# Performance work log

Hardware: AMD Instinct MI355X
Metric: run time of the kernel (lower is better)

The kernel has to match this reference:

```python
import jax, jax.numpy as jnp
import numpy as np

NEG = -9e15  # mask value used by dense GAT-style implementations
ALPHA = 0.1  # leaky_relu negative slope (init arg)
DENSITY = 0.05  # sparsity of the incidence/adjacency operator


def setup_inputs() -> dict:
    key = jax.random.key(0)
    ks = jax.random.split(key, 7)
    n_s, n_t = 8192, 4096
    s_in = t_in = 128
    s_out = t_out = 64
    H = 4
    input1 = jax.random.normal(ks[0], (n_s, s_in), dtype=jnp.float32)
    input2 = jax.random.normal(ks[1], (n_t, t_in), dtype=jnp.float32)
    A_opt = (jax.random.uniform(ks[2], (n_t, n_s)) < DENSITY).astype(jnp.float32)
    # per-head params, stacked on leading head axis (math identical to num_heads separate layers)
    Ws = jax.random.normal(ks[3], (H, s_in, t_out), dtype=jnp.float32) * (1.0 / np.sqrt(s_in))
    Wt = jax.random.normal(ks[4], (H, t_in, s_out), dtype=jnp.float32) * (1.0 / np.sqrt(t_in))
    a_src = jax.random.normal(ks[5], (H, t_out), dtype=jnp.float32) * 0.1
    a_tgt = jax.random.normal(ks[6], (H, s_out), dtype=jnp.float32) * 0.1
    return {"input1": input1, "input2": input2, "A_opt": A_opt,
            "Ws": Ws, "Wt": Wt, "a_src": a_src, "a_tgt": a_tgt}


def _forward(input1, input2, A_opt, Ws, Wt, a_src, a_tgt):
    # hs: source feats projected to target_out space; ht: target feats -> source_out space
    hs = jnp.einsum('si,hio->hso', input1, Ws)          # [H, n_s, t_out]
    ht = jnp.einsum('ti,hio->hto', input2, Wt)          # [H, n_t, s_out]
    # additive GAT score, broadcast over the [n_t, n_s] grid
    e = jax.nn.leaky_relu(
        jnp.einsum('hto,ho->ht', ht, a_tgt)[:, :, None]
        + jnp.einsum('hso,ho->hs', hs, a_src)[:, None, :],
        negative_slope=ALPHA)                            # [H, n_t, n_s]
    mask = (A_opt != 0.0)[None]                          # [1, n_t, n_s]
    e_masked = jnp.where(mask, e, NEG)
    attn_ts = jax.nn.softmax(e_masked, axis=-1)          # normalize over source cells
    attn_st = jax.nn.softmax(e_masked, axis=-2)          # normalize over target cells
    h_ts = jax.nn.elu(jnp.einsum('hts,hso->hto', attn_ts, hs))  # [H, n_t, t_out]
    h_st = jax.nn.elu(jnp.einsum('hts,hto->hso', attn_st, ht))  # [H, n_s, s_out]
    # concatenate heads along feature dim (concatenate=True)
    out_st = jnp.transpose(h_st, (1, 0, 2)).reshape(input1.shape[0], -1)  # [n_s, H*s_out]
    out_ts = jnp.transpose(h_ts, (1, 0, 2)).reshape(input2.shape[0], -1)  # [n_t, H*t_out]
    return out_st, out_ts


def reference(input1, input2, A_opt, Ws, Wt, a_src, a_tgt):
    return _forward(input1, input2, A_opt, Ws, Wt, a_src, a_tgt)
```

## Files before the change

### kernel.cpp

```cpp
#include <hip/hip_runtime.h>
#include <hip/hip_bf16.h>

#define H 4
#define NS 8192
#define NT 4096
#define DIN 128
#define DOUT 64
#define ROW_CAP 1024
#define COL_CAP 512
#define NEGBIG -3.0e38f

typedef unsigned uint4_vt __attribute__((ext_vector_type(4)));

__device__ __forceinline__ float lrelu(float x) { return x >= 0.f ? x : 0.1f * x; }
__device__ __forceinline__ float eluf(float x) { return x > 0.f ? x : expm1f(x); }

__device__ __forceinline__ float waveMax(float v) {
    for (int off = 32; off > 0; off >>= 1) v = fmaxf(v, __shfl_xor(v, off, 64));
    return v;
}
__device__ __forceinline__ float waveSum(float v) {
    for (int off = 32; off > 0; off >>= 1) v += __shfl_xor(v, off, 64);
    return v;
}
__device__ __forceinline__ float rlane(float v, int l) {
    return __int_as_float(__builtin_amdgcn_readlane(__float_as_int(v), l));
}

__global__ __launch_bounds__(256) void proj_kernel(
    const float* __restrict__ X, const float* __restrict__ W,
    const float* __restrict__ a_vec, float* __restrict__ Hout,
    float* __restrict__ b_out, int N) {
    __shared__ float w_lds[DIN * DOUT];
    __shared__ float a_lds[16 * 129];
    const int h = blockIdx.y;
    const int row0 = blockIdx.x * 16;
    const int tid = threadIdx.x;

    const float* Wh = W + (size_t)h * DIN * DOUT;
    for (int i = tid; i < DIN * DOUT; i += 256) w_lds[i] = Wh[i];
    for (int i = tid; i < 16 * DIN; i += 256) {
        int r = i >> 7, c = i & 127;
        a_lds[r * 129 + c] = X[(size_t)(row0 + r) * DIN + c];
    }
    __syncthreads();

    const int fg = (tid & 15) * 4;
    const int r = tid >> 4;
    const float* ar = &a_lds[r * 129];
    float acc0 = 0.f, acc1 = 0.f, acc2 = 0.f, acc3 = 0.f;
#pragma unroll 8
    for (int i = 0; i < DIN; ++i) {
        float av = ar[i];
        float4 wv = *reinterpret_cast<const float4*>(&w_lds[i * DOUT + fg]);
        acc0 += av * wv.x; acc1 += av * wv.y; acc2 += av * wv.z; acc3 += av * wv.w;
    }
    const int s = row0 + r;
    float4 o = make_float4(acc0, acc1, acc2, acc3);
    *reinterpret_cast<float4*>(&Hout[((size_t)h * N + s) * DOUT + fg]) = o;

    const float* av = a_vec + h * DOUT + fg;
    float part = acc0 * av[0] + acc1 * av[1] + acc2 * av[2] + acc3 * av[3];
    for (int off = 8; off > 0; off >>= 1) part += __shfl_xor(part, off, 64);
    if ((tid & 15) == 0) b_out[(size_t)h * N + s] = part;
}

__global__ __launch_bounds__(256) void mask_kernel(
    const float* __restrict__ A,
    unsigned long long* __restrict__ mask_row,
    unsigned long long* __restrict__ mask_col) {
    __shared__ unsigned long long rowbits[64];
    const int s0 = blockIdx.x * 64;
    const int t0 = blockIdx.y * 64;
    const int lane = threadIdx.x & 63;
    const int w = threadIdx.x >> 6;
    for (int rr = w; rr < 64; rr += 4) {
        const int t = t0 + rr;
        float v = A[(size_t)t * NS + s0 + lane];
        unsigned long long word = __ballot(v != 0.0f);
        if (lane == 0) {
            mask_row[(size_t)t * (NS / 64) + (s0 >> 6)] = word;
            rowbits[rr] = word;
        }
    }
    __syncthreads();
    if (threadIdx.x < 64) {
        const int j = threadIdx.x;
        unsigned long long cw = 0;
        for (int rr = 0; rr < 64; ++rr) cw |= ((rowbits[rr] >> j) & 1ull) << rr;
        mask_col[(size_t)(s0 + j) * (NT / 64) + (t0 >> 6)] = cw;
    }
}

template <int NWORDS, int CAP>
__device__ __forceinline__ int wave_compact(
    const unsigned long long* __restrict__ mask, size_t word_base,
    unsigned* list, int lane) {
    int total = 0;
#pragma unroll
    for (int c = 0; c < NWORDS / 64; ++c) {
        unsigned long long wd = mask[word_base + c * 64 + lane];
        int cnt = __popcll(wd);
        int incl = cnt;
#pragma unroll
        for (int d = 1; d < 64; d <<= 1) {
            int v = __shfl_up(incl, d, 64);
            if (lane >= d) incl += v;
        }
        int off = total + incl - cnt;
        const unsigned base = (unsigned)(c * 64 + lane) * 64u;
        while (wd) {
            int b = __ffsll((long long)wd) - 1;
            if (off < CAP) list[off] = (base + (unsigned)b) << 8;
            ++off;
            wd &= wd - 1;
        }
        total += __shfl(incl, 63, 64);
    }
    int nnz = total > CAP ? CAP : total;
    int nk64 = (nnz + 63) & ~63;
    for (int j = nnz + lane; j < nk64; j += 64) list[j] = 0;
    return nnz;
}

template <int KMAX>
__device__ __forceinline__ float attn_core(
    const unsigned* __restrict__ list, int nnz,
    const float* __restrict__ bvec,
    float bias,
    const float* __restrict__ src,
    int lane) {
    const int nk = (nnz + 63) >> 6;
    float wreg[KMAX];

    float m = NEGBIG;
#pragma unroll
    for (int k = 0; k < KMAX; ++k) {
        if (k >= nk) break;
        int j = (k << 6) + lane;
        float p = NEGBIG;
        if (j < nnz) p = bvec[list[j] >> 8];
        wreg[k] = p;
        m = fmaxf(m, p);
    }
    m = waveMax(m);
    const float mrow = lrelu(bias + m);

    float ssum = 0.f;
#pragma unroll
    for (int k = 0; k < KMAX; ++k) {
        if (k >= nk) break;
        int j = (k << 6) + lane;
        float w = 0.f;
        if (j < nnz) w = __expf(lrelu(bias + wreg[k]) - mrow);
        wreg[k] = w;
        ssum += w;
    }
    ssum = waveSum(ssum);
    const float rs = ssum > 0.f ? 1.0f / ssum : 0.f;

    const char* srcb = (const char*)src;
    const unsigned laneoff = (unsigned)lane << 2;
    float a0 = 0.f, a1 = 0.f, a2 = 0.f, a3 = 0.f;
    float a4 = 0.f, a5 = 0.f, a6 = 0.f, a7 = 0.f;
#pragma unroll
    for (int k = 0; k < KMAX; ++k) {
        if (k >= nk) break;
        const float wk = wreg[k];
        const uint4_vt* lp = reinterpret_cast<const uint4_vt*>(&list[k << 6]);
#pragma unroll
        for (int g = 0; g < 16; g += 2) {
            uint4_vt i0 = lp[g];
            uint4_vt i1 = lp[g + 1];
            const int l = g << 2;
            a0 += rlane(wk, l + 0) * *(const float*)(srcb + (i0[0] + laneoff));
            a1 += rlane(wk, l + 1) * *(const float*)(srcb + (i0[1] + laneoff));
            a2 += rlane(wk, l + 2) * *(const float*)(srcb + (i0[2] + laneoff));
            a3 += rlane(wk, l + 3) * *(const float*)(srcb + (i0[3] + laneoff));
            a4 += rlane(wk, l + 4) * *(const float*)(srcb + (i1[0] + laneoff));
            a5 += rlane(wk, l + 5) * *(const float*)(srcb + (i1[1] + laneoff));
            a6 += rlane(wk, l + 6) * *(const float*)(srcb + (i1[2] + laneoff));
            a7 += rlane(wk, l + 7) * *(const float*)(srcb + (i1[3] + laneoff));
        }
    }
    float acc = ((a0 + a1) + (a2 + a3)) + ((a4 + a5) + (a6 + a7));
    return acc * rs;
}

__global__ __launch_bounds__(256) void attn_row_kernel(
    const unsigned long long* __restrict__ mask_row,
    const float* __restrict__ bs, const float* __restrict__ bt,
    const float* __restrict__ hs, float* __restrict__ out_ts) {
    __shared__ __align__(16) unsigned list[4][ROW_CAP];

    const int bid = blockIdx.x;
    const int w = threadIdx.x >> 6, lane = threadIdx.x & 63;
    const int h = (bid & 7) >> 1;
    const int tgroup = ((bid >> 3) << 1) | (bid & 1);
    const int t = tgroup * 4 + w;

    const int nnz = wave_compact<NS / 64, ROW_CAP>(
        mask_row, (size_t)t * (NS / 64), list[w], lane);

    const float btv = bt[(size_t)h * NT + t];
    float r = attn_core<ROW_CAP / 64>(list[w], nnz, bs + (size_t)h * NS, btv,
                                      hs + (size_t)h * NS * DOUT, lane);
    out_ts[(size_t)t * (H * DOUT) + h * DOUT + lane] = eluf(r);
}

__global__ __launch_bounds__(256) void attn_col_kernel(
    const unsigned long long* __restrict__ mask_col,
    const float* __restrict__ bs, const float* __restrict__ bt,
    const float* __restrict__ ht, float* __restrict__ out_st) {
    __shared__ __align__(16) unsigned list[4][COL_CAP];

    const int bid = blockIdx.x;
    const int w = threadIdx.x >> 6, lane = threadIdx.x & 63;
    const int h = (bid & 7) >> 1;
    const int sgroup = ((bid >> 3) << 1) | (bid & 1);
    const int s = sgroup * 4 + w;

    const int nnz = wave_compact<NT / 64, COL_CAP>(
        mask_col, (size_t)s * (NT / 64), list[w], lane);

    const float bsv = bs[(size_t)h * NS + s];
    float r = attn_core<COL_CAP / 64>(list[w], nnz, bt + (size_t)h * NT, bsv,
                                      ht + (size_t)h * NT * DOUT, lane);
    out_st[(size_t)s * (H * DOUT) + h * DOUT + lane] = eluf(r);
}

extern "C" void kernel_launch(void* const* d_in, const int* in_sizes, int n_in,
                              void* d_out, int out_size, void* d_ws, size_t ws_size,
                              hipStream_t stream) {
    const float* input1 = (const float*)d_in[0];
    const float* input2 = (const float*)d_in[1];
    const float* A      = (const float*)d_in[2];
    const float* Ws     = (const float*)d_in[3];
    const float* Wt     = (const float*)d_in[4];
    const float* a_src  = (const float*)d_in[5];
    const float* a_tgt  = (const float*)d_in[6];
    float* out = (float*)d_out;

    char* ws = (char*)d_ws;
    float* hs = (float*)(ws + 0);
    float* ht = (float*)(ws + 8388608);
    float* bs = (float*)(ws + 12582912);
    float* bt = (float*)(ws + 12713984);
    unsigned long long* mask_row = (unsigned long long*)(ws + 12779520);
    unsigned long long* mask_col = (unsigned long long*)(ws + 16973824);

    proj_kernel<<<dim3(NS / 16, H), 256, 0, stream>>>(input1, Ws, a_src, hs, bs, NS);
    proj_kernel<<<dim3(NT / 16, H), 256, 0, stream>>>(input2, Wt, a_tgt, ht, bt, NT);
    mask_kernel<<<dim3(NS / 64, NT / 64), 256, 0, stream>>>(A, mask_row, mask_col);
    attn_row_kernel<<<NT * H / 4, 256, 0, stream>>>(mask_row, bs, bt, hs,
                                                    out + (size_t)NS * (H * DOUT));
    attn_col_kernel<<<NS * H / 4, 256, 0, stream>>>(mask_col, bs, bt, ht, out);
}
```

Baseline: 410.7 us.

## Gather float4 feature rows per quarter-wave and fuse row/col attention launches

Rewrites the sparse attention gather so each quarter-wave of 16 lanes loads one neighbour's 64-float feature row as float4 vectors. Four neighbours are handled per step, with a cross-quarter shuffle reduction at the end, instead of one scalar load per lane per neighbour with readlane weight broadcasts. The row and column attention kernels are merged into one launch that branches on block index, removing a launch and letting both halves run concurrently. This trades fewer, wider memory transactions for extra shuffles, and the fused kernel always reserves the larger shared list size, which may lower occupancy for column blocks.

New measurement: 390.5 us. 4.9% less time.

```diff
diff --git a/kernel.cpp b/kernel.cpp
--- a/kernel.cpp
+++ b/kernel.cpp
@@ -10,8 +10,6 @@
 #define COL_CAP 512
 #define NEGBIG -3.0e38f
 
-typedef unsigned uint4_vt __attribute__((ext_vector_type(4)));
-
 __device__ __forceinline__ float lrelu(float x) { return x >= 0.f ? x : 0.1f * x; }
 __device__ __forceinline__ float eluf(float x) { return x > 0.f ? x : expm1f(x); }
 
@@ -22,9 +20,6 @@
 __device__ __forceinline__ float waveSum(float v) {
     for (int off = 32; off > 0; off >>= 1) v += __shfl_xor(v, off, 64);
     return v;
-}
-__device__ __forceinline__ float rlane(float v, int l) {
-    return __int_as_float(__builtin_amdgcn_readlane(__float_as_int(v), l));
 }
 
 __global__ __launch_bounds__(256) void proj_kernel(
@@ -124,12 +119,11 @@
 }
 
 template <int KMAX>
-__device__ __forceinline__ float attn_core(
+__device__ __forceinline__ void attn_gather4(
     const unsigned* __restrict__ list, int nnz,
-    const float* __restrict__ bvec,
-    float bias,
-    const float* __restrict__ src,
-    int lane) {
+    const float* __restrict__ bvec, float bias,
+    const char* __restrict__ srcb, int lane,
+    float& rs_out, float4& acc_out) {
     const int nk = (nnz + 63) >> 6;
     float wreg[KMAX];
 
@@ -157,76 +151,85 @@
         ssum += w;
     }
     ssum = waveSum(ssum);
-    const float rs = ssum > 0.f ? 1.0f / ssum : 0.f;
-
-    const char* srcb = (const char*)src;
-    const unsigned laneoff = (unsigned)lane << 2;
-    float a0 = 0.f, a1 = 0.f, a2 = 0.f, a3 = 0.f;
-    float a4 = 0.f, a5 = 0.f, a6 = 0.f, a7 = 0.f;
+    rs_out = ssum > 0.f ? 1.0f / ssum : 0.f;
+
+    const int qsel = lane >> 4;
+    const unsigned lane16 = (unsigned)(lane & 15) << 4;
+    float4 acc = make_float4(0.f, 0.f, 0.f, 0.f);
 #pragma unroll
     for (int k = 0; k < KMAX; ++k) {
         if (k >= nk) break;
         const float wk = wreg[k];
-        const uint4_vt* lp = reinterpret_cast<const uint4_vt*>(&list[k << 6]);
-#pragma unroll
-        for (int g = 0; g < 16; g += 2) {
-            uint4_vt i0 = lp[g];
-            uint4_vt i1 = lp[g + 1];
-            const int l = g << 2;
-            a0 += rlane(wk, l + 0) * *(const float*)(srcb + (i0[0] + laneoff));
-            a1 += rlane(wk, l + 1) * *(const float*)(srcb + (i0[1] + laneoff));
-            a2 += rlane(wk, l + 2) * *(const float*)(srcb + (i0[2] + laneoff));
-            a3 += rlane(wk, l + 3) * *(const float*)(srcb + (i0[3] + laneoff));
-            a4 += rlane(wk, l + 4) * *(const float*)(srcb + (i1[0] + laneoff));
-            a5 += rlane(wk, l + 5) * *(const float*)(srcb + (i1[1] + laneoff));
-            a6 += rlane(wk, l + 6) * *(const float*)(srcb + (i1[2] + laneoff));
-            a7 += rlane(wk, l + 7) * *(const float*)(srcb + (i1[3] + laneoff));
-        }
-    }
-    float acc = ((a0 + a1) + (a2 + a3)) + ((a4 + a5) + (a6 + a7));
-    return acc * rs;
-}
-
-__global__ __launch_bounds__(256) void attn_row_kernel(
+        const unsigned* lk = list + (k << 6);
+#pragma unroll 4
+        for (int kk = 0; kk < 16; ++kk) {
+            const int e = (kk << 2) + qsel;
+            unsigned off = lk[e];
+            float w = __shfl(wk, e, 64);
+            const float4 v = *reinterpret_cast<const float4*>(srcb + (off + lane16));
+            acc.x += w * v.x; acc.y += w * v.y;
+            acc.z += w * v.z; acc.w += w * v.w;
+        }
+    }
+#pragma unroll
+    for (int mx = 16; mx < 64; mx <<= 1) {
+        acc.x += __shfl_xor(acc.x, mx, 64);
+        acc.y += __shfl_xor(acc.y, mx, 64);
+        acc.z += __shfl_xor(acc.z, mx, 64);
+        acc.w += __shfl_xor(acc.w, mx, 64);
+    }
+    acc_out = acc;
+}
+
+__global__ __launch_bounds__(256) void attn_fused_kernel(
     const unsigned long long* __restrict__ mask_row,
+    const unsigned long long* __restrict__ mask_col,
     const float* __restrict__ bs, const float* __restrict__ bt,
-    const float* __restrict__ hs, float* __restrict__ out_ts) {
+    const float* __restrict__ hs, const float* __restrict__ ht,
+    float* __restrict__ out_st, float* __restrict__ out_ts) {
     __shared__ __align__(16) unsigned list[4][ROW_CAP];
 
     const int bid = blockIdx.x;
     const int w = threadIdx.x >> 6, lane = threadIdx.x & 63;
-    const int h = (bid & 7) >> 1;
-    const int tgroup = ((bid >> 3) << 1) | (bid & 1);
-    const int t = tgroup * 4 + w;
-
-    const int nnz = wave_compact<NS / 64, ROW_CAP>(
-        mask_row, (size_t)t * (NS / 64), list[w], lane);
-
-    const float btv = bt[(size_t)h * NT + t];
-    float r = attn_core<ROW_CAP / 64>(list[w], nnz, bs + (size_t)h * NS, btv,
-                                      hs + (size_t)h * NS * DOUT, lane);
-    out_ts[(size_t)t * (H * DOUT) + h * DOUT + lane] = eluf(r);
-}
-
-__global__ __launch_bounds__(256) void attn_col_kernel(
-    const unsigned long long* __restrict__ mask_col,
-    const float* __restrict__ bs, const float* __restrict__ bt,
-    const float* __restrict__ ht, float* __restrict__ out_st) {
-    __shared__ __align__(16) unsigned list[4][COL_CAP];
-
-    const int bid = blockIdx.x;
-    const int w = threadIdx.x >> 6, lane = threadIdx.x & 63;
-    const int h = (bid & 7) >> 1;
-    const int sgroup = ((bid >> 3) << 1) | (bid & 1);
-    const int s = sgroup * 4 + w;
-
-    const int nnz = wave_compact<NT / 64, COL_CAP>(
-        mask_col, (size_t)s * (NT / 64), list[w], lane);
-
-    const float bsv = bs[(size_t)h * NS + s];
-    float r = attn_core<COL_CAP / 64>(list[w], nnz, bt + (size_t)h * NT, bsv,
-                                      ht + (size_t)h * NT * DOUT, lane);
-    out_st[(size_t)s * (H * DOUT) + h * DOUT + lane] = eluf(r);
+
+    if (bid < NT * H / 4) {
+        const int h = (bid & 7) >> 1;
+        const int tgroup = ((bid >> 3) << 1) | (bid & 1);
+        const int t = tgroup * 4 + w;
+        const int nnz = wave_compact<NS / 64, ROW_CAP>(
+            mask_row, (size_t)t * (NS / 64), list[w], lane);
+        float rs; float4 acc;
+        attn_gather4<ROW_CAP / 64>(list[w], nnz, bs + (size_t)h * NS,
+                                   bt[(size_t)h * NT + t],
+                                   (const char*)(hs + (size_t)h * NS * DOUT),
+                                   lane, rs, acc);
+        if (lane < 16) {
+            float4 o;
+            o.x = eluf(acc.x * rs); o.y = eluf(acc.y * rs);
+            o.z = eluf(acc.z * rs); o.w = eluf(acc.w * rs);
+            *reinterpret_cast<float4*>(
+                &out_ts[(size_t)t * (H * DOUT) + h * DOUT + lane * 4]) = o;
+        }
+    } else {
+        const int b2 = bid - NT * H / 4;
+        const int h = (b2 & 7) >> 1;
+        const int sgroup = ((b2 >> 3) << 1) | (b2 & 1);
+        const int s = sgroup * 4 + w;
+        const int nnz = wave_compact<NT / 64, COL_CAP>(
+            mask_col, (size_t)s * (NT / 64), list[w], lane);
+        float rs; float4 acc;
+        attn_gather4<COL_CAP / 64>(list[w], nnz, bt + (size_t)h * NT,
+                                   bs[(size_t)h * NS + s],
+                                   (const char*)(ht + (size_t)h * NT * DOUT),
+                                   lane, rs, acc);
+        if (lane < 16) {
+            float4 o;
+            o.x = eluf(acc.x * rs); o.y = eluf(acc.y * rs);
+            o.z = eluf(acc.z * rs); o.w = eluf(acc.w * rs);
+            *reinterpret_cast<float4*>(
+                &out_st[(size_t)s * (H * DOUT) + h * DOUT + lane * 4]) = o;
+        }
+    }
 }
 
 extern "C" void kernel_launch(void* const* d_in, const int* in_sizes, int n_in,
@@ -252,7 +255,7 @@
     proj_kernel<<<dim3(NS / 16, H), 256, 0, stream>>>(input1, Ws, a_src, hs, bs, NS);
     proj_kernel<<<dim3(NT / 16, H), 256, 0, stream>>>(input2, Wt, a_tgt, ht, bt, NT);
     mask_kernel<<<dim3(NS / 64, NT / 64), 256, 0, stream>>>(A, mask_row, mask_col);
-    attn_row_kernel<<<NT * H / 4, 256, 0, stream>>>(mask_row, bs, bt, hs,
-                                                    out + (size_t)NS * (H * DOUT));
-    attn_col_kernel<<<NS * H / 4, 256, 0, stream>>>(mask_col, bs, bt, ht, out);
-}
+    attn_fused_kernel<<<(NT * H + NS * H) / 4, 256, 0, stream>>>(
+        mask_row, mask_col, bs, bt, hs, ht,
+        out, out + (size_t)NS * (H * DOUT));
+}
```
